# Kernel tuning notes

Measured on AMD Instinct MI355X. Metric: run time of the kernel, lower is better.

Reference implementation:

```python
import jax, jax.numpy as jnp
import numpy as np

T, N, HID = 128, 128, 64
H_, W_ = 8, 8
CONV_OUT = H_ * W_ * HID  # 4096
N_SUB = 5
A, B, C = 5, 3, 6          # subtask_space = task_space.nvec[0]
SUB_SIZE = A + B + C       # 14
N_G = A * B * C            # 90
STATE = N_SUB + SUB_SIZE + HID + SUB_SIZE + 1 + 1  # 99
D_IN = CONV_OUT + 3 * N_SUB  # 4111


def setup_inputs() -> dict:
    key = jax.random.key(0)
    ks = jax.random.split(key, 16)
    sc = 0.02
    obs = jax.random.normal(ks[0], (T, N, CONV_OUT), jnp.float32)
    task_type = jax.random.randint(ks[1], (T, N, N_SUB), 0, A).astype(jnp.float32)
    count = jax.random.randint(ks[2], (T, N, N_SUB), 1, B + 1).astype(jnp.float32)
    obj = jax.random.randint(ks[3], (T, N, N_SUB), 0, C).astype(jnp.float32)
    inp = jnp.concatenate([obs, task_type, count, obj], axis=-1)  # [T,N,4111]
    hx = jnp.zeros((1, N, STATE), jnp.float32)
    return {
        "input": inp,
        "hx": hx,
        "Wf": jax.random.normal(ks[4], (HID, CONV_OUT + 2 * SUB_SIZE + 1), jnp.float32) * sc,
        "bf": jnp.zeros((HID,), jnp.float32),
        "Wih": jax.random.normal(ks[5], (3 * HID, 2 * HID), jnp.float32) * sc,
        "bih": jnp.zeros((3 * HID,), jnp.float32),
        "bhh": jnp.zeros((3 * HID,), jnp.float32),
        "Wc": jax.random.normal(ks[6], (1, 2 * HID), jnp.float32) * sc,
        "bc": jnp.zeros((1,), jnp.float32),
        "Wl": jax.random.normal(ks[7], (3, HID), jnp.float32) * sc,
        "bl": jnp.zeros((3,), jnp.float32),
        "Wpi": jax.random.normal(ks[8], (N_G, HID + SUB_SIZE), jnp.float32) * sc,
        "bpi": jnp.zeros((N_G,), jnp.float32),
        "Wb": jax.random.normal(ks[9], (2, CONV_OUT + SUB_SIZE), jnp.float32) * sc,
        "bb": jnp.zeros((2,), jnp.float32),
    }


def _forward(input, hx, Wf, bf, Wih, bih, bhh, Wc, bc, Wl, bl, Wpi, bpi, Wb, bb):
    obs = input[..., :CONV_OUT]
    tt = input[..., CONV_OUT:CONV_OUT + N_SUB].astype(jnp.int32)
    cnt = input[..., CONV_OUT + N_SUB:CONV_OUT + 2 * N_SUB].astype(jnp.int32) - 1
    obj = input[..., CONV_OUT + 2 * N_SUB:].astype(jnp.int32)

    ea, eb, ec = jnp.eye(A, dtype=input.dtype), jnp.eye(B, dtype=input.dtype), jnp.eye(C, dtype=input.dtype)

    def embed(t1, t2, t3):
        return jnp.concatenate([ea[t1], eb[t2], ec[t3]], axis=-1)

    M = embed(tt[0], cnt[0], obj[0])  # [N, N_SUB, SUB_SIZE]

    # parse hidden state
    h0_all = hx[0]
    i0, i1, i2, i3, i4 = np.cumsum([N_SUB, SUB_SIZE, HID, SUB_SIZE, 1])
    p0, r0, h0, g0, b0 = (h0_all[:, :i0], h0_all[:, i0:i1], h0_all[:, i1:i2],
                          h0_all[:, i2:i3], h0_all[:, i3:i4])

    new_ep = jnp.all(hx == 0)
    p0 = jnp.where(new_ep, p0.at[:, 0].set(1.0), p0)
    r0 = jnp.where(new_ep, M[:, 0], r0)
    g0 = jnp.where(new_ep, M[:, 0], g0)

    bhr, bhz, bhn = jnp.split(bhh, 3)
    keys = jax.random.split(jax.random.key(42), input.shape[0])

    def step(carry, xs):
        p_, r_, h_, g_, bprev = carry
        x, k = xs
        s = jnp.concatenate([x, r_, g_, bprev], axis=-1) @ Wf.T + bf   # f (linear)
        sh = jnp.concatenate([s, h_], axis=-1)
        cg = jax.nn.sigmoid(sh @ Wc.T + bc)                             # [N,1] phi_update
        # GRUCell called with hidden=None -> zero hidden state
        gi = sh @ Wih.T + bih
        gr, gz, gn = jnp.split(gi, 3, axis=-1)
        rg = jax.nn.sigmoid(gr + bhr)
        z = jax.nn.sigmoid(gz + bhz)
        n = jnp.tanh(gn + rg * bhn)
        hnew = (1.0 - z) * n
        # shift attention: per-batch conv1d(p, l, padding=1)
        l = jax.nn.softmax(h_ @ Wl.T + bl, axis=-1)                     # [N,3]
        pp = jnp.pad(p_, ((0, 0), (1, 1)))
        pconv = pp[:, :-2] * l[:, :1] + pp[:, 1:-1] * l[:, 1:2] + pp[:, 2:] * l[:, 2:]
        rnew = jnp.einsum('nk,nks->ns', pconv, M)
        p = cg * pconv + (1.0 - cg) * p_
        r = cg * rnew + (1.0 - cg) * r_
        h = cg * hnew + (1.0 - cg) * h_
        # pi_theta categorical over prod(subtask_space)
        lg = jnp.concatenate([h, r], axis=-1) @ Wpi.T + bpi
        k1, k2 = jax.random.split(k)
        g_idx = jax.random.categorical(k1, lg)                          # [N]
        lp_g = jnp.take_along_axis(jax.nn.log_softmax(lg, axis=-1), g_idx[:, None], axis=1)
        t1 = g_idx // (B * C)
        rem = g_idx % (B * C)
        gemb = embed(t1, rem // C, rem % C)                             # [N, SUB_SIZE]
        g = cg * gemb + (1.0 - cg) * g_
        # beta categorical over 2
        lbeta = jnp.concatenate([x, g], axis=-1) @ Wb.T + bb
        b_idx = jax.random.categorical(k2, lbeta)
        lp_b = jnp.take_along_axis(jax.nn.log_softmax(lbeta, axis=-1), b_idx[:, None], axis=1)
        bflt = b_idx[:, None].astype(p.dtype)
        out = jnp.concatenate([p, r, h, g, bflt, lp_g + lp_b], axis=-1)  # [N, STATE]
        return (p, r, h, g, bflt), out

    _, outs = jax.lax.scan(step, (p0, r0, h0, g0, b0), (obs, keys))
    return outs  # [T, N, STATE]


def reference(input, hx, Wf, bf, Wih, bih, bhh, Wc, bc, Wl, bl, Wpi, bpi, Wb, bb):
    outs = _forward(input, hx, Wf, bf, Wih, bih, bhh, Wc, bc, Wl, bl, Wpi, bpi, Wb, bb)
    return outs, outs[-1]
```

## Files before the change

### kernel.cpp

```cpp
#include <hip/hip_runtime.h>
#include <stdint.h>
#include <math.h>

#define T_STEPS 128
#define NB      128
#define HID     64
#define CONVOUT 4096
#define NSUB    5
#define SUBSZ   14
#define NG      90
#define STATE   99
#define DIN     4111
#define WFCOLS  4125
#define WBCOLS  4110
#define NROWS   (T_STEPS * NB)
#define GIXST   193

#define NEGINFF (-3.0e38f)

typedef __attribute__((ext_vector_type(2))) float f32x2;

#define SEL5(a,b,c,d,e,ix) ((ix)==0?(a):(ix)==1?(b):(ix)==2?(c):(ix)==3?(d):(e))
#define SEL3(a,b,c,ix)     ((ix)==0?(a):(ix)==1?(b):(c))
#define SEL6(a,b,c,d,e,f,ix) ((ix)==0?(a):(ix)==1?(b):(ix)==2?(c):(ix)==3?(d):(ix)==4?(e):(f))
// ... 225 lines not shown
  float* o = GIx + (size_t)row * GIXST + i0;
  #pragma unroll
  for (int j = 0; j < 48; ++j) o[j] = acc[j];
  if (w == 3) o[48] = acc48;
}

__global__ void k_noise(double* __restrict__ Gg, double* __restrict__ Gb) {
  int b = blockIdx.x;
  int t = b / 9, c = b - t * 9;
  int tid = threadIdx.x;
  unsigned a, bk, k1a, k1b, k2a, k2b, o0, o1;
  tf2x32(0u, 42u, 0u, (unsigned)t, a, bk);
  if (c < 8) {
    tf2x32(a, bk, 0u, 0u, k1a, k1b);
    int i0 = c * 1440;
    for (int i = i0 + tid; i < i0 + 1440; i += 256) {
      tf2x32(k1a, k1b, 0u, (unsigned)i, o0, o1);
      Gg[(size_t)t * NB * NG + i] = bits_to_gumbel_d(o0 ^ o1);
    }
  } else {
    tf2x32(a, bk, 0u, 1u, k2a, k2b);
    tf2x32(k2a, k2b, 0u, (unsigned)tid, o0, o1);
    Gb[(size_t)t * NB * 2 + tid] = bits_to_gumbel_d(o0 ^ o1);
  }
}

__global__ __launch_bounds__(256, 1) void k_scan(
    const float* __restrict__ inp, const float* __restrict__ hx,
    const float* __restrict__ Wf,
    const float* __restrict__ Wih, const float* __restrict__ bih,
    const float* __restrict__ bhh, const float* __restrict__ Wc,
    const float* __restrict__ bc, const float* __restrict__ Wl,
    const float* __restrict__ bl, const float* __restrict__ Wpi,
    const float* __restrict__ bpi, const float* __restrict__ Wb,
    const float* __restrict__ bb,
    const float* __restrict__ GIx, const double* __restrict__ Xb,
    const double* __restrict__ Gg, const double* __restrict__ Gb,
    float* __restrict__ lgst, float* __restrict__ lbst,
    int* __restrict__ gidxst, int* __restrict__ bidxst,
    float* __restrict__ out) {
  const int n = blockIdx.x;
  const int tid = threadIdx.x;
  const int lane = tid & 63;
  const int w = __builtin_amdgcn_readfirstlane(tid >> 6);

  __shared__ __align__(16) float h_lds[64];
  __shared__ __align__(16) float gi_lds[192];
  __shared__ float pq_lds[4];
  __shared__ float cp_lds[2][8];
  __shared__ float pm_lds[3][2];
  __shared__ int   pidx_lds[3];
  __shared__ int   pub_i[4];
  __shared__ float pub_f[2];
  __shared__ int   nz_sh;
  __shared__ float ws_lds[29][64];
  __shared__ float rg0_lds[32];
  __shared__ int   ti_lds[16];

  const int i = tid - 64;
  const int oi = (w >= 1) ? (w - 1) * 30 + lane : 0;

  f32x2 wih_h[32];
  f32x2 wpi_p[32];
  float bihc = 0.f, bpi_r = 0.f;
  float Mg[14], V[5], WpiM[5];
  float m_b = 0.f, GI_r = 0.f, GI_g = 0.f, accR = 0.f, gihreg = 0.f;
  float gixA = 0.f;
  double gumA = 0.0, gumB = 0.0;
  #pragma unroll
  for (int j = 0; j < 14; ++j) Mg[j] = 0.f;
  #pragma unroll
  for (int k = 0; k < 5; ++k) { V[k] = 0.f; WpiM[k] = 0.f; }

  float rgbp = 0.f, hreg = 0.f;
  float mtr[5];
  float bhr_r = 0, bhz_r = 0, bhn_r = 0;
  float wc0 = 0, wc1 = 0, wl0 = 0, wl1 = 0, wl2 = 0;
  float bl0 = 0, bl1 = 0, bl2 = 0, bc0 = 0;
  float wbs0 = 0, wbs1 = 0;
  float kap[5], wg[14], wcB = 0.f;
  float cR = 0.f, cG = 0.f, CXa = 0.f;
  double S0 = 0.0, S1 = 0.0, bb0d = 0.0, bb1d = 0.0;
  double xb0 = 0.0, xb1 = 0.0, gb0 = 0.0, gb1 = 0.0;
  double xb0n = 0.0, xb1n = 0.0, gb0n = 0.0, gb1n = 0.0;
  int dsto = -1;
  int ttk[5], cnk[5], obk[5];
  float wfs[29];
  #pragma unroll
  for (int k = 0; k < 5; ++k) { mtr[k] = 0.f; kap[k] = 0.f; ttk[k] = 0; cnk[k] = 0; obk[k] = 0; }
  #pragma unroll
  for (int j = 0; j < 14; ++j) wg[j] = 0.f;
  #pragma unroll
  for (int k = 0; k < 29; ++k) wfs[k] = 0.f;

  if (tid == 0) nz_sh = 0;
  __syncthreads();
  {
    int any = 0;
    const float4* h4 = (const float4*)hx;
    for (int q = tid; q < (NB * STATE) / 4; q += 256) {
      float4 v = h4[q];
      any |= (v.x != 0.f) | (v.y != 0.f) | (v.z != 0.f) | (v.w != 0.f);
    }
    if (any) nz_sh = 1;
  }
  if (w == 0) {
    #pragma unroll
    for (int k = 0; k < 29; ++k) wfs[k] = Wf[(size_t)lane * WFCOLS + CONVOUT + k];
    bhr_r = bhh[lane]; bhz_r = bhh[64 + lane]; bhn_r = bhh[128 + lane];
    wc0 = Wc[lane]; wc1 = Wc[64 + lane]; bc0 = bc[0];
    wl0 = Wl[lane]; wl1 = Wl[64 + lane]; wl2 = Wl[128 + lane];
    bl0 = bl[0]; bl1 = bl[1]; bl2 = bl[2];
    bb0d = (double)bb[0]; bb1d = (double)bb[1];
    if (lane < 14) { wbs0 = Wb[CONVOUT + lane]; wbs1 = Wb[(size_t)WBCOLS + CONVOUT + lane]; }
    const float* r0 = inp + (size_t)n * DIN + CONVOUT;
    #pragma unroll
    for (int k = 0; k < 5; ++k) {
      int ttv = (int)r0[k], cntv = (int)r0[5 + k] - 1, objv = (int)r0[10 + k];
      ttk[k] = ttv; cnk[k] = cntv; obk[k] = objv;
      float v = 0.f;
      if (lane < 5)       v = (lane == ttv) ? 1.f : 0.f;
      else if (lane < 8)  v = ((lane - 5) == cntv) ? 1.f : 0.f;
      else if (lane < 14) v = ((lane - 8) == objv) ? 1.f : 0.f;
      mtr[k] = v;
      if (lane == 0) { ti_lds[k] = ttv; ti_lds[5 + k] = cntv; ti_lds[10 + k] = objv; }
    }
    int src = -1;
    if (lane < 14)       { dsto = 5 + lane;          src = dsto; }
    else if (lane < 28)  { dsto = 83 + (lane - 14);  src = dsto; }
    else if (lane == 28) { dsto = 97;                src = 97; }
    else if (lane < 34)  { dsto = lane - 29;         src = dsto; }
    rgbp = (src >= 0) ? hx[(size_t)n * STATE + src] : 0.f;
    hreg = hx[(size_t)n * STATE + 19 + lane];
  }
  __syncthreads();

  if (w == 0) {
    if (nz_sh == 0) {
      if (lane == 29) rgbp = 1.f;
      else if (lane < 14) rgbp = mtr[0];
      else if (lane >= 14 && lane < 28) {
        int j = lane - 14;
        rgbp = (j < 5) ? ((j == ttk[0]) ? 1.f : 0.f)
             : (j < 8) ? (((j - 5) == cnk[0]) ? 1.f : 0.f)
                       : (((j - 8) == obk[0]) ? 1.f : 0.f);
      }
    }
    #pragma unroll
    for (int j = 0; j < 29; ++j) ws_lds[j][lane] = wfs[j];
    if (lane < 28) rg0_lds[lane] = rgbp;
    if (lane == 28) { rg0_lds[28] = rgbp; pub_f[0] = rgbp; }
    h_lds[lane] = hreg;
    if (lane < 6) cp_lds[1][lane] = 0.f;
    if (lane < 3) pub_i[lane] = 0;
  }
  __syncthreads();

  if (w == 0) {
    #pragma unroll
    for (int k = 0; k < 5; ++k) {
      float wfrm = SEL5(wfs[0], wfs[1], wfs[2], wfs[3], wfs[4], ttk[k])
                 + SEL3(wfs[5], wfs[6], wfs[7], cnk[k])
                 + SEL6(wfs[8], wfs[9], wfs[10], wfs[11], wfs[12], wfs[13], obk[k]);
      kap[k] = dpp_sum_bcast(wc0 * wfrm);
    }
    #pragma unroll
    for (int j = 0; j < 14; ++j) wg[j] = dpp_sum_bcast(wc0 * wfs[14 + j]);
    wcB = dpp_sum_bcast(wc0 * wfs[28]);
    {
      float rs = 0.f, gs = 0.f;
      #pragma unroll
      for (int j = 0; j < 14; ++j) {
        rs = fmaf(wfs[j], rlane(rgbp, j), rs);
        gs = fmaf(wfs[14 + j], rlane(rgbp, 14 + j), gs);
      }
      cR = dpp_sum_bcast(wc0 * rs);
      cG = dpp_sum_bcast(wc0 * gs);
    }
    #pragma unroll
    for (int j = 0; j < 14; ++j) {
      double gv = (double)rlane(rgbp, 14 + j);
      S0 += gv * (double)rlane(wbs0, j);
      S1 += gv * (double)rlane(wbs1, j);
    }
    CXa = GIx[((size_t)0 * NB + n) * GIXST + 192];
    xb0 = Xb[(size_t)n * 2 + 0]; xb1 = Xb[(size_t)n * 2 + 1];
    gb0 = Gb[(size_t)n * 2 + 0]; gb1 = Gb[(size_t)n * 2 + 1];
    float p0 = wl0 * hreg, p1 = wl1 * hreg, p2 = wl2 * hreg, cah = wc1 * hreg;
    dpp_sum4(p0, p1, p2, cah);
    if (lane == 63) { pq_lds[0] = p0; pq_lds[1] = p1; pq_lds[2] = p2; pq_lds[3] = cah; }
  } else {
    float Mr[14];
    #pragma unroll
    for (int j = 0; j < 14; ++j) Mr[j] = 0.f;
    {
      float wsrow[64];
      {
        const f32x2* wr0 = (const f32x2*)&Wih[(size_t)i * 128];
        #pragma unroll
        for (int l2 = 0; l2 < 32; ++l2) { f32x2 v = wr0[l2]; wsrow[2*l2] = v.x; wsrow[2*l2+1] = v.y; }
      }
      #pragma unroll
      for (int l = 0; l < 64; ++l) {
        float wv = wsrow[l];
        #pragma unroll
        for (int j = 0; j < 14; ++j) {
          Mr[j] = fmaf(wv, ws_lds[j][l], Mr[j]);
          Mg[j] = fmaf(wv, ws_lds[14 + j][l], Mg[j]);
        }
        m_b = fmaf(wv, ws_lds[28][l], m_b);
      }
    }
    #pragma unroll
    for (int k = 0; k < 5; ++k) {
      int tt = ti_lds[k], cn = ti_lds[5 + k], ob = ti_lds[10 + k];
      V[k] = SEL5(Mr[0], Mr[1], Mr[2], Mr[3], Mr[4], tt)
           + SEL3(Mr[5], Mr[6], Mr[7], cn)
           + SEL6(Mr[8], Mr[9], Mr[10], Mr[11], Mr[12], Mr[13], ob);
    }
    GI_r = 0.f; GI_g = 0.f;
    #pragma unroll
    for (int j = 0; j < 14; ++j) {
      GI_r = fmaf(Mr[j], rg0_lds[j], GI_r);
      GI_g = fmaf(Mg[j], rg0_lds[14 + j], GI_g);
    }
    {
      const f32x2* wr = (const f32x2*)&Wih[(size_t)i * 128 + 64];
      #pragma unroll
      for (int k2 = 0; k2 < 32; ++k2) wih_h[k2] = wr[k2];
      bihc = bih[i];
    }
    if (lane < 30) {
      const f32x2* pr = (const f32x2*)&Wpi[(size_t)oi * 78];
      #pragma unroll
      for (int k2 = 0; k2 < 32; ++k2) wpi_p[k2] = pr[k2];
      bpi_r = bpi[oi];
      const float* wp = Wpi + (size_t)oi * 78 + 64;
      #pragma unroll
      for (int k = 0; k < 5; ++k)
        WpiM[k] = wp[ti_lds[k]] + wp[5 + ti_lds[5 + k]] + wp[8 + ti_lds[10 + k]];
      accR = 0.f;
      #pragma unroll
      for (int j = 0; j < 14; ++j) accR = fmaf(wp[j], rg0_lds[j], accR);
      gumA = Gg[(size_t)n * NG + oi];
    }
    gixA = GIx[((size_t)0 * NB + n) * GIXST + i];
    {
      const f32x2* hp = (const f32x2*)h_lds;
      f32x2 A = {bihc, 0.f}, B = {0.f, 0.f};
      #pragma unroll
      for (int k2 = 0; k2 < 32; k2 += 2) {
        f32x2 h0 = hp[k2], h1 = hp[k2 + 1];
        A.x = fmaf(wih_h[k2].x, h0.x, A.x);
        A.y = fmaf(wih_h[k2].y, h0.y, A.y);
        B.x = fmaf(wih_h[k2 + 1].x, h1.x, B.x);
        B.y = fmaf(wih_h[k2 + 1].y, h1.y, B.y);
      }
      gihreg = (A.x + A.y) + (B.x + B.y);
    }
  }
  __syncthreads();

  const size_t outF = (size_t)T_STEPS * NB * STATE;

  float cg = 0.f;
  double cgd = 0.0;

  #pragma unroll 1
  for (int t = 0; t < T_STEPS; ++t) {
    if (w == 0) {
      float P0 = pq_lds[0] + bl0, P1v = pq_lds[1] + bl1, P2v = pq_lds[2] + bl2;
      float cgaH = pq_lds[3];
      float mx = fmaxf(P0, fmaxf(P1v, P2v));
      float e0 = expf(P0 - mx), e1 = expf(P1v - mx), e2 = expf(P2v - mx);
      float se = e0 + e1 + e2;
      float l0 = e0 / se, l1 = e1 / se, l2 = e2 / se;
      float bprev = rlane(rgbp, 28);
      float cga = CXa + cR + cG + bprev * wcB + cgaH;
      cg = 1.f / (1.f + expf(-(cga + bc0)));
      cgd = (double)cg;
      float pv0 = rlane(rgbp, 29), pv1 = rlane(rgbp, 30), pv2 = rlane(rgbp, 31);
      float pv3 = rlane(rgbp, 32), pv4 = rlane(rgbp, 33);
      float pc0 = pv0 * l1 + pv1 * l2;
      float pc1 = pv0 * l0 + pv1 * l1 + pv2 * l2;
      float pc2 = pv1 * l0 + pv2 * l1 + pv3 * l2;
      float pc3 = pv2 * l0 + pv3 * l1 + pv4 * l2;
      float pc4 = pv3 * l0 + pv4 * l1;
      if (lane >= 29 && lane < 34) {
        float pcl = (lane == 29) ? pc0 : (lane == 30) ? pc1 : (lane == 31) ? pc2
                  : (lane == 32) ? pc3 : pc4;
        rgbp = cg * pcl + (1.f - cg) * rgbp;
      }
      if (lane < 14) {
        float rn2 = pc0 * mtr[0] + pc1 * mtr[1] + pc2 * mtr[2] + pc3 * mtr[3] + pc4 * mtr[4];
        rgbp = cg * rn2 + (1.f - cg) * rgbp;
      }
      cR = cg * (pc0 * kap[0] + pc1 * kap[1] + pc2 * kap[2] + pc3 * kap[3] + pc4 * kap[4])
         + (1.f - cg) * cR;
      if (lane == 0) {
        float* cp = cp_lds[t & 1];
        cp[0] = cg; cp[1] = pc0; cp[2] = pc1; cp[3] = pc2; cp[4] = pc3; cp[5] = pc4;
      }
    } else {
      const float* cp = cp_lds[(t + 1) & 1];
      float cgp = cp[0];
      float rmix = cp[1] * V[0] + cp[2] * V[1] + cp[3] * V[2] + cp[4] * V[3] + cp[5] * V[4];
      GI_r = cgp * rmix + (1.f - cgp) * GI_r;
      int pt1 = pub_i[0], pb1 = pub_i[1], pc1i = pub_i[2];
      float mgs = SEL5(Mg[0], Mg[1], Mg[2], Mg[3], Mg[4], pt1)
                + SEL3(Mg[5], Mg[6], Mg[7], pb1)
                + SEL6(Mg[8], Mg[9], Mg[10], Mg[11], Mg[12], Mg[13], pc1i);
      GI_g = cgp * mgs + (1.f - cgp) * GI_g;
      float bprev = pub_f[0];
      gi_lds[i] = gihreg + gixA + GI_r + GI_g + bprev * m_b;
    }
    bar_lds();

    if (w == 0) {
      float g0 = gi_lds[lane], g1 = gi_lds[64 + lane], g2 = gi_lds[128 + lane];
      float rg = 1.f / (1.f + expf(-(g0 + bhr_r)));
      float z  = 1.f / (1.f + expf(-(g1 + bhz_r)));
      float nn = tanhf(g2 + rg * bhn_r);
      hreg = cg * ((1.f - z) * nn) + (1.f - cg) * hreg;
      h_lds[lane] = hreg;
    } else {
      int tn = (t + 1 < T_STEPS) ? t + 1 : t;
      gixA = GIx[((size_t)tn * NB + n) * GIXST + i];
      if (lane < 30) gumB = Gg[(size_t)tn * NB * NG + (size_t)n * NG + oi];
    }
    bar_lds();

    if (w != 0) {
      const float* cp = cp_lds[t & 1];
      float cgc = cp[0];
      float vb = NEGINFF;
      if (lane < 30) {
        float rmx = cp[1] * WpiM[0] + cp[2] * WpiM[1] + cp[3] * WpiM[2]
                  + cp[4] * WpiM[3] + cp[5] * WpiM[4];
        accR = cgc * rmx + (1.f - cgc) * accR;
        const f32x2* hp = (const f32x2*)h_lds;
        f32x2 A = {bpi_r + accR, 0.f}, B = {0.f, 0.f};
        #pragma unroll
        for (int k2 = 0; k2 < 32; k2 += 2) {
          f32x2 h0 = hp[k2], h1 = hp[k2 + 1];
          A.x = fmaf(wpi_p[k2].x, h0.x, A.x);
          A.y = fmaf(wpi_p[k2].y, h0.y, A.y);
          B.x = fmaf(wpi_p[k2 + 1].x, h1.x, B.x);
          B.y = fmaf(wpi_p[k2 + 1].y, h1.y, B.y);
        }
        float lgv = (A.x + A.y) + (B.x + B.y);
        lgst[((size_t)t * NB + n) * NG + oi] = lgv;
        vb = (float)(gumA + (double)lgv);
      }
      gumA = gumB;
      float m1 = vb, m2 = NEGINFF;
      dpp_amax2(m1, m2);
      float M1w = rlane(m1, 63);
      unsigned long long bm = __ballot(vb == M1w);
      int il = __ffsll(bm) - 1;
      if (lane == 63) { pm_lds[w - 1][0] = m1; pm_lds[w - 1][1] = m2; pidx_lds[w - 1] = il; }
    } else {
      float p0 = wl0 * hreg, p1 = wl1 * hreg, p2 = wl2 * hreg, cah = wc1 * hreg;
      dpp_sum4(p0, p1, p2, cah);
      if (lane == 63) { pq_lds[0] = p0; pq_lds[1] = p1; pq_lds[2] = p2; pq_lds[3] = cah; }
      size_t rn = (size_t)t * NB + n;
      float* ob = out + rn * STATE;
      ob[19 + lane] = hreg;
      if (dsto >= 0 && (lane < 14 || lane >= 29)) ob[dsto] = rgbp;
      int tn = (t + 1 < T_STEPS) ? t + 1 : t;
      CXa = GIx[((size_t)tn * NB + n) * GIXST + 192];
      xb0n = Xb[((size_t)tn * NB + n) * 2 + 0];
      xb1n = Xb[((size_t)tn * NB + n) * 2 + 1];
      gb0n = Gb[((size_t)tn * NB + n) * 2 + 0];
      gb1n = Gb[((size_t)tn * NB + n) * 2 + 1];
    }
    bar_lds();

    if (w == 0) {
      float m1a = pm_lds[0][0], m2a = pm_lds[0][1];
      float m1b = pm_lds[1][0], m2b = pm_lds[1][1];
      float m1c = pm_lds[2][0], m2c = pm_lds[2][1];
      float M1 = fmaxf(m1a, fmaxf(m1b, m1c));
      float M2; int gidx;
      if (m1a == M1)      { M2 = fmaxf(m2a, fmaxf(m1b, m1c)); gidx = pidx_lds[0]; }
      else if (m1b == M1) { M2 = fmaxf(m2b, fmaxf(m1a, m1c)); gidx = 30 + pidx_lds[1]; }
      else                { M2 = fmaxf(m2c, fmaxf(m1a, m1b)); gidx = 60 + pidx_lds[2]; }
      if (M1 - M2 < 3e-5f) {
        double gum0s = Gg[(size_t)t * NB * NG + (size_t)n * NG + lane];
        double gum1s = (lane < 26) ? Gg[(size_t)t * NB * NG + (size_t)n * NG + 64 + lane] : 0.0;
        double e0d = (double)bpi[lane];
        double e1d = (lane < 26) ? (double)bpi[64 + lane] : -1.0e300;
        #pragma unroll 1
        for (int k = 0; k < 64; ++k) {
          double hv2 = (double)rlane(hreg, k);
          e0d = fma((double)Wpi[(size_t)lane * 78 + k], hv2, e0d);
          if (lane < 26) e1d = fma((double)Wpi[(size_t)(64 + lane) * 78 + k], hv2, e1d);
        }
        #pragma unroll 1
        for (int k = 0; k < 14; ++k) {
          double rv = (double)rlane(rgbp, k);
          e0d = fma((double)Wpi[(size_t)lane * 78 + 64 + k], rv, e0d);
          if (lane < 26) e1d = fma((double)Wpi[(size_t)(64 + lane) * 78 + 64 + k], rv, e1d);
        }
        double kk0 = e0d + gum0s;
        double kk1 = (lane < 26) ? e1d + gum1s : -1.0e300;
        double d1; int di;
        if (kk1 > kk0) { d1 = kk1; di = lane + 64; } else { d1 = kk0; di = lane; }
        #pragma unroll
        for (int off = 32; off; off >>= 1) {
          double od = __shfl_xor(d1, off, 64);
          int    oid = __shfl_xor(di, off, 64);
          if (od > d1 || (od == d1 && oid < di)) { d1 = od; di = oid; }
        }
        gidx = di;
      }
      int t1 = gidx / 18, rem = gidx - t1 * 18;
      int b1 = rem / 6, c1 = rem - b1 * 6;
      if (lane >= 14 && lane < 28) {
        int j = lane - 14;
        float ge = (j < 5) ? ((j == t1) ? 1.f : 0.f)
                 : (j < 8) ? (((j - 5) == b1) ? 1.f : 0.f)
                           : (((j - 8) == c1) ? 1.f : 0.f);
        rgbp = cg * ge + (1.f - cg) * rgbp;
      }
      float wgs = SEL5(wg[0], wg[1], wg[2], wg[3], wg[4], t1)
                + SEL3(wg[5], wg[6], wg[7], b1)
                + SEL6(wg[8], wg[9], wg[10], wg[11], wg[12], wg[13], c1);
      cG = cg * wgs + (1.f - cg) * cG;
      double u0 = (double)rlane(wbs0, t1) + (double)rlane(wbs0, 5 + b1) + (double)rlane(wbs0, 8 + c1);
      double u1 = (double)rlane(wbs1, t1) + (double)rlane(wbs1, 5 + b1) + (double)rlane(wbs1, 8 + c1);
      S0 = cgd * u0 + (1.0 - cgd) * S0;
      S1 = cgd * u1 + (1.0 - cgd) * S1;
      double lb0 = xb0 + bb0d + S0;
      double lb1 = xb1 + bb1d + S1;
      int bi = ((lb1 + gb1) > (lb0 + gb0)) ? 1 : 0;
      if (lane == 28) rgbp = (float)bi;
      size_t rn = (size_t)t * NB + n;
      float* ob = out + rn * STATE;
      if (dsto >= 0 && lane >= 14 && lane < 29) ob[dsto] = rgbp;
      if (lane == 0) {
        lbst[rn * 2 + 0] = (float)lb0; lbst[rn * 2 + 1] = (float)lb1;
        gidxst[rn] = gidx; bidxst[rn] = bi;
        pub_i[0] = t1; pub_i[1] = b1; pub_i[2] = c1;
      }
      if (lane == 28) pub_f[0] = rgbp;
      if (t == T_STEPS - 1) {
        float* of = out + outF + (size_t)n * STATE;
        if (dsto >= 0) of[dsto] = rgbp;
        of[19 + lane] = hreg;
      }
      xb0 = xb0n; xb1 = xb1n; gb0 = gb0n; gb1 = gb1n;
    } else {
      const f32x2* hp = (const f32x2*)h_lds;
      f32x2 A = {bihc, 0.f}, B = {0.f, 0.f};
      #pragma unroll
      for (int k2 = 0; k2 < 32; k2 += 2) {
        f32x2 h0 = hp[k2], h1 = hp[k2 + 1];
        A.x = fmaf(wih_h[k2].x, h0.x, A.x);
        A.y = fmaf(wih_h[k2].y, h0.y, A.y);
        B.x = fmaf(wih_h[k2 + 1].x, h1.x, B.x);
        B.y = fmaf(wih_h[k2 + 1].y, h1.y, B.y);
      }
      gihreg = (A.x + A.y) + (B.x + B.y);
    }
    bar_lds();
  }
}

__global__ __launch_bounds__(256) void k_lp(const float* __restrict__ lgst,
                                            const float* __restrict__ lbst,
                                            const int* __restrict__ gidxst,
                                            const int* __restrict__ bidxst,
                                            float* __restrict__ out) {
  int tid = threadIdx.x, lane = tid & 63, w = tid >> 6;
  size_t rn = (size_t)blockIdx.x * 4 + w;
  const float* lg = lgst + rn * NG;
  float v0 = lg[lane];
  float v1 = (lane < 26) ? lg[64 + lane] : -3.0e38f;
  float ml = fmaxf(v0, v1);
  #pragma unroll
  for (int off = 32; off; off >>= 1) ml = fmaxf(ml, __shfl_xor(ml, off, 64));
  float e = expf(v0 - ml) + ((lane < 26) ? expf(v1 - ml) : 0.f);
  #pragma unroll
  for (int off = 32; off; off >>= 1) e += __shfl_xor(e, off, 64);
  int gi = gidxst[rn];
  float lpg = (lg[gi] - ml) - logf(e);
  float lb0 = lbst[rn * 2 + 0], lb1 = lbst[rn * 2 + 1];
  int bi = bidxst[rn];
  float mx = fmaxf(lb0, lb1);
  float seb = expf(lb0 - mx) + expf(lb1 - mx);
  float lpb = ((bi ? lb1 : lb0) - mx) - logf(seb);
  if (lane == 0) {
    int t = (int)(rn / NB), n = (int)(rn % NB);
    float lp = lpg + lpb;
    out[rn * STATE + 98] = lp;
    if (t == T_STEPS - 1) out[(size_t)T_STEPS * NB * STATE + (size_t)n * STATE + 98] = lp;
  }
}

extern "C" void kernel_launch(void* const* d_in, const int* in_sizes, int n_in,
                              void* d_out, int out_size, void* d_ws, size_t ws_size,
                              hipStream_t stream) {
  const float* inp = (const float*)d_in[0];
  const float* hx  = (const float*)d_in[1];
  const float* Wf  = (const float*)d_in[2];
  const float* bf  = (const float*)d_in[3];
  const float* Wih = (const float*)d_in[4];
  const float* bih = (const float*)d_in[5];
  const float* bhh = (const float*)d_in[6];
  const float* Wc  = (const float*)d_in[7];
  const float* bc  = (const float*)d_in[8];
  const float* Wl  = (const float*)d_in[9];
  const float* bl  = (const float*)d_in[10];
  const float* Wpi = (const float*)d_in[11];
  const float* bpi = (const float*)d_in[12];
  const float* Wb  = (const float*)d_in[13];
  const float* bb  = (const float*)d_in[14];
  float* out = (float*)d_out;
// ... 30 lines not shown
```

Before: 940.6 us.

## Split recurrent loop into per-wave role loops and drop hx scan barrier

Restructures the sequential recurrence kernel so that wave 0 and the worker waves each run their own specialized time loop with matching barrier counts. Per-role state is scoped to its own branch, which is meant to cut register pressure and remove the per-step wave-uniform branching. The hx nonzero scan now runs in wave 0 only and uses a ballot instead of a shared flag, so one block-wide sync disappears. The risk is that the barrier sequences of the two loops fall out of step, which would deadlock or corrupt results, and the hx scan now runs on 64 threads instead of 256.

```diff
diff --git a/kernel.cpp b/kernel.cpp
--- a/kernel.cpp
+++ b/kernel.cpp
@@ -301,59 +301,38 @@
   __shared__ int   pidx_lds[3];
   __shared__ int   pub_i[4];
   __shared__ float pub_f[2];
-  __shared__ int   nz_sh;
   __shared__ float ws_lds[29][64];
   __shared__ float rg0_lds[32];
   __shared__ int   ti_lds[16];
 
-  const int i = tid - 64;
-  const int oi = (w >= 1) ? (w - 1) * 30 + lane : 0;
-
-  f32x2 wih_h[32];
-  f32x2 wpi_p[32];
-  float bihc = 0.f, bpi_r = 0.f;
-  float Mg[14], V[5], WpiM[5];
-  float m_b = 0.f, GI_r = 0.f, GI_g = 0.f, accR = 0.f, gihreg = 0.f;
-  float gixA = 0.f;
-  double gumA = 0.0, gumB = 0.0;
-  #pragma unroll
-  for (int j = 0; j < 14; ++j) Mg[j] = 0.f;
-  #pragma unroll
-  for (int k = 0; k < 5; ++k) { V[k] = 0.f; WpiM[k] = 0.f; }
-
-  float rgbp = 0.f, hreg = 0.f;
-  float mtr[5];
-  float bhr_r = 0, bhz_r = 0, bhn_r = 0;
-  float wc0 = 0, wc1 = 0, wl0 = 0, wl1 = 0, wl2 = 0;
-  float bl0 = 0, bl1 = 0, bl2 = 0, bc0 = 0;
-  float wbs0 = 0, wbs1 = 0;
-  float kap[5], wg[14], wcB = 0.f;
-  float cR = 0.f, cG = 0.f, CXa = 0.f;
-  double S0 = 0.0, S1 = 0.0, bb0d = 0.0, bb1d = 0.0;
-  double xb0 = 0.0, xb1 = 0.0, gb0 = 0.0, gb1 = 0.0;
-  double xb0n = 0.0, xb1n = 0.0, gb0n = 0.0, gb1n = 0.0;
-  int dsto = -1;
-  int ttk[5], cnk[5], obk[5];
-  float wfs[29];
-  #pragma unroll
-  for (int k = 0; k < 5; ++k) { mtr[k] = 0.f; kap[k] = 0.f; ttk[k] = 0; cnk[k] = 0; obk[k] = 0; }
-  #pragma unroll
-  for (int j = 0; j < 14; ++j) wg[j] = 0.f;
-  #pragma unroll
-  for (int k = 0; k < 29; ++k) wfs[k] = 0.f;
-
-  if (tid == 0) nz_sh = 0;
-  __syncthreads();
-  {
-    int any = 0;
-    const float4* h4 = (const float4*)hx;
-    for (int q = tid; q < (NB * STATE) / 4; q += 256) {
-      float4 v = h4[q];
-      any |= (v.x != 0.f) | (v.y != 0.f) | (v.z != 0.f) | (v.w != 0.f);
-    }
-    if (any) nz_sh = 1;
-  }
+  const size_t outF = (size_t)T_STEPS * NB * STATE;
+
   if (w == 0) {
+    float rgbp = 0.f, hreg = 0.f;
+    float mtr[5];
+    float bhr_r, bhz_r, bhn_r;
+    float wc0, wc1, wl0, wl1, wl2;
+    float bl0, bl1, bl2, bc0;
+    float wbs0 = 0.f, wbs1 = 0.f;
+    float kap[5], wg[14], wcB;
+    float cR, cG, CXa;
+    double S0 = 0.0, S1 = 0.0, bb0d, bb1d;
+    double xb0, xb1, gb0, gb1;
+    double xb0n, xb1n, gb0n, gb1n;
+    int dsto = -1;
+    int ttk[5], cnk[5], obk[5];
+    float wfs[29];
+
+    bool nz;
+    {
+      int any = 0;
+      const float4* h4 = (const float4*)hx;
+      for (int q = lane; q < (NB * STATE) / 4; q += 64) {
+        float4 v = h4[q];
+        any |= (v.x != 0.f) | (v.y != 0.f) | (v.z != 0.f) | (v.w != 0.f);
+      }
+      nz = (__ballot(any) != 0ULL);
+    }
     #pragma unroll
     for (int k = 0; k < 29; ++k) wfs[k] = Wf[(size_t)lane * WFCOLS + CONVOUT + k];
     bhr_r = bhh[lane]; bhz_r = bhh[64 + lane]; bhn_r = bhh[128 + lane];
@@ -362,30 +341,30 @@
     bl0 = bl[0]; bl1 = bl[1]; bl2 = bl[2];
     bb0d = (double)bb[0]; bb1d = (double)bb[1];
     if (lane < 14) { wbs0 = Wb[CONVOUT + lane]; wbs1 = Wb[(size_t)WBCOLS + CONVOUT + lane]; }
-    const float* r0 = inp + (size_t)n * DIN + CONVOUT;
-    #pragma unroll
-    for (int k = 0; k < 5; ++k) {
-      int ttv = (int)r0[k], cntv = (int)r0[5 + k] - 1, objv = (int)r0[10 + k];
-      ttk[k] = ttv; cnk[k] = cntv; obk[k] = objv;
-      float v = 0.f;
-      if (lane < 5)       v = (lane == ttv) ? 1.f : 0.f;
-      else if (lane < 8)  v = ((lane - 5) == cntv) ? 1.f : 0.f;
-      else if (lane < 14) v = ((lane - 8) == objv) ? 1.f : 0.f;
-      mtr[k] = v;
-      if (lane == 0) { ti_lds[k] = ttv; ti_lds[5 + k] = cntv; ti_lds[10 + k] = objv; }
-    }
-    int src = -1;
-    if (lane < 14)       { dsto = 5 + lane;          src = dsto; }
-    else if (lane < 28)  { dsto = 83 + (lane - 14);  src = dsto; }
-    else if (lane == 28) { dsto = 97;                src = 97; }
-    else if (lane < 34)  { dsto = lane - 29;         src = dsto; }
-    rgbp = (src >= 0) ? hx[(size_t)n * STATE + src] : 0.f;
-    hreg = hx[(size_t)n * STATE + 19 + lane];
-  }
-  __syncthreads();
-
-  if (w == 0) {
-    if (nz_sh == 0) {
+    {
+      const float* r0 = inp + (size_t)n * DIN + CONVOUT;
+      #pragma unroll
+      for (int k = 0; k < 5; ++k) {
+        int ttv = (int)r0[k], cntv = (int)r0[5 + k] - 1, objv = (int)r0[10 + k];
+        ttk[k] = ttv; cnk[k] = cntv; obk[k] = objv;
+        float v = 0.f;
+        if (lane < 5)       v = (lane == ttv) ? 1.f : 0.f;
+        else if (lane < 8)  v = ((lane - 5) == cntv) ? 1.f : 0.f;
+        else if (lane < 14) v = ((lane - 8) == objv) ? 1.f : 0.f;
+        mtr[k] = v;
+        if (lane == 0) { ti_lds[k] = ttv; ti_lds[5 + k] = cntv; ti_lds[10 + k] = objv; }
+      }
+    }
+    {
+      int src = -1;
+      if (lane < 14)       { dsto = 5 + lane;          src = dsto; }
+      else if (lane < 28)  { dsto = 83 + (lane - 14);  src = dsto; }
+      else if (lane == 28) { dsto = 97;                src = 97; }
+      else if (lane < 34)  { dsto = lane - 29;         src = dsto; }
+      rgbp = (src >= 0) ? hx[(size_t)n * STATE + src] : 0.f;
+      hreg = hx[(size_t)n * STATE + 19 + lane];
+    }
+    if (!nz) {
       if (lane == 29) rgbp = 1.f;
       else if (lane < 14) rgbp = mtr[0];
       else if (lane >= 14 && lane < 28) {
@@ -402,10 +381,9 @@
     h_lds[lane] = hreg;
     if (lane < 6) cp_lds[1][lane] = 0.f;
     if (lane < 3) pub_i[lane] = 0;
-  }
-  __syncthreads();
-
-  if (w == 0) {
+
+    bar_lds();
+
     #pragma unroll
     for (int k = 0; k < 5; ++k) {
       float wfrm = SEL5(wfs[0], wfs[1], wfs[2], wfs[3], wfs[4], ttk[k])
@@ -435,43 +413,213 @@
     CXa = GIx[((size_t)0 * NB + n) * GIXST + 192];
     xb0 = Xb[(size_t)n * 2 + 0]; xb1 = Xb[(size_t)n * 2 + 1];
     gb0 = Gb[(size_t)n * 2 + 0]; gb1 = Gb[(size_t)n * 2 + 1];
-    float p0 = wl0 * hreg, p1 = wl1 * hreg, p2 = wl2 * hreg, cah = wc1 * hreg;
-    dpp_sum4(p0, p1, p2, cah);
-    if (lane == 63) { pq_lds[0] = p0; pq_lds[1] = p1; pq_lds[2] = p2; pq_lds[3] = cah; }
+    xb0n = xb0; xb1n = xb1; gb0n = gb0; gb1n = gb1;
+    {
+      float p0 = wl0 * hreg, p1 = wl1 * hreg, p2 = wl2 * hreg, cah = wc1 * hreg;
+      dpp_sum4(p0, p1, p2, cah);
+      if (lane == 63) { pq_lds[0] = p0; pq_lds[1] = p1; pq_lds[2] = p2; pq_lds[3] = cah; }
+    }
+
+    bar_lds();
+
+    float cg = 0.f;
+    double cgd = 0.0;
+
+    #pragma unroll 1
+    for (int t = 0; t < T_STEPS; ++t) {
+      {
+        float P0 = pq_lds[0] + bl0, P1v = pq_lds[1] + bl1, P2v = pq_lds[2] + bl2;
+        float cgaH = pq_lds[3];
+        float mx = fmaxf(P0, fmaxf(P1v, P2v));
+        float e0 = expf(P0 - mx), e1 = expf(P1v - mx), e2 = expf(P2v - mx);
+        float se = e0 + e1 + e2;
+        float l0 = e0 / se, l1 = e1 / se, l2 = e2 / se;
+        float bprev = rlane(rgbp, 28);
+        float cga = CXa + cR + cG + bprev * wcB + cgaH;
+        cg = 1.f / (1.f + expf(-(cga + bc0)));
+        cgd = (double)cg;
+        float pv0 = rlane(rgbp, 29), pv1 = rlane(rgbp, 30), pv2 = rlane(rgbp, 31);
+        float pv3 = rlane(rgbp, 32), pv4 = rlane(rgbp, 33);
+        float pc0 = pv0 * l1 + pv1 * l2;
+        float pc1 = pv0 * l0 + pv1 * l1 + pv2 * l2;
+        float pc2 = pv1 * l0 + pv2 * l1 + pv3 * l2;
+        float pc3 = pv2 * l0 + pv3 * l1 + pv4 * l2;
+        float pc4 = pv3 * l0 + pv4 * l1;
+        if (lane >= 29 && lane < 34) {
+          float pcl = (lane == 29) ? pc0 : (lane == 30) ? pc1 : (lane == 31) ? pc2
+                    : (lane == 32) ? pc3 : pc4;
+          rgbp = cg * pcl + (1.f - cg) * rgbp;
+        }
+        if (lane < 14) {
+          float rn2 = pc0 * mtr[0] + pc1 * mtr[1] + pc2 * mtr[2] + pc3 * mtr[3] + pc4 * mtr[4];
+          rgbp = cg * rn2 + (1.f - cg) * rgbp;
+        }
+        cR = cg * (pc0 * kap[0] + pc1 * kap[1] + pc2 * kap[2] + pc3 * kap[3] + pc4 * kap[4])
+           + (1.f - cg) * cR;
+        if (lane == 0) {
+          float* cp = cp_lds[t & 1];
+          cp[0] = cg; cp[1] = pc0; cp[2] = pc1; cp[3] = pc2; cp[4] = pc3; cp[5] = pc4;
+        }
+      }
+      bar_lds();
+
+      {
+        float g0 = gi_lds[lane], g1 = gi_lds[64 + lane], g2 = gi_lds[128 + lane];
+        float rg = 1.f / (1.f + expf(-(g0 + bhr_r)));
+        float z  = 1.f / (1.f + expf(-(g1 + bhz_r)));
+        float nn = tanhf(g2 + rg * bhn_r);
+        hreg = cg * ((1.f - z) * nn) + (1.f - cg) * hreg;
+        h_lds[lane] = hreg;
+      }
+      bar_lds();
+
+      {
+        float p0 = wl0 * hreg, p1 = wl1 * hreg, p2 = wl2 * hreg, cah = wc1 * hreg;
+        dpp_sum4(p0, p1, p2, cah);
+        if (lane == 63) { pq_lds[0] = p0; pq_lds[1] = p1; pq_lds[2] = p2; pq_lds[3] = cah; }
+        size_t rn = (size_t)t * NB + n;
+        float* ob = out + rn * STATE;
+        ob[19 + lane] = hreg;
+        if (dsto >= 0 && (lane < 14 || lane >= 29)) ob[dsto] = rgbp;
+        int tn = (t + 1 < T_STEPS) ? t + 1 : t;
+        CXa = GIx[((size_t)tn * NB + n) * GIXST + 192];
+        xb0n = Xb[((size_t)tn * NB + n) * 2 + 0];
+        xb1n = Xb[((size_t)tn * NB + n) * 2 + 1];
+        gb0n = Gb[((size_t)tn * NB + n) * 2 + 0];
+        gb1n = Gb[((size_t)tn * NB + n) * 2 + 1];
+      }
+      bar_lds();
+
+      {
+        float m1a = pm_lds[0][0], m2a = pm_lds[0][1];
+        float m1b = pm_lds[1][0], m2b = pm_lds[1][1];
+        float m1c = pm_lds[2][0], m2c = pm_lds[2][1];
+        float M1 = fmaxf(m1a, fmaxf(m1b, m1c));
+        float M2; int gidx;
+        if (m1a == M1)      { M2 = fmaxf(m2a, fmaxf(m1b, m1c)); gidx = pidx_lds[0]; }
+        else if (m1b == M1) { M2 = fmaxf(m2b, fmaxf(m1a, m1c)); gidx = 30 + pidx_lds[1]; }
+        else                { M2 = fmaxf(m2c, fmaxf(m1a, m1b)); gidx = 60 + pidx_lds[2]; }
+        if (M1 - M2 < 3e-5f) {
+          double gum0s = Gg[(size_t)t * NB * NG + (size_t)n * NG + lane];
+          double gum1s = (lane < 26) ? Gg[(size_t)t * NB * NG + (size_t)n * NG + 64 + lane] : 0.0;
+          double e0d = (double)bpi[lane];
+          double e1d = (lane < 26) ? (double)bpi[64 + lane] : -1.0e300;
+          #pragma unroll 1
+          for (int k = 0; k < 64; ++k) {
+            double hv2 = (double)rlane(hreg, k);
+            e0d = fma((double)Wpi[(size_t)lane * 78 + k], hv2, e0d);
+            if (lane < 26) e1d = fma((double)Wpi[(size_t)(64 + lane) * 78 + k], hv2, e1d);
+          }
+          #pragma unroll 1
+          for (int k = 0; k < 14; ++k) {
+            double rv = (double)rlane(rgbp, k);
+            e0d = fma((double)Wpi[(size_t)lane * 78 + 64 + k], rv, e0d);
+            if (lane < 26) e1d = fma((double)Wpi[(size_t)(64 + lane) * 78 + 64 + k], rv, e1d);
+          }
+          double kk0 = e0d + gum0s;
+          double kk1 = (lane < 26) ? e1d + gum1s : -1.0e300;
+          double d1; int di;
+          if (kk1 > kk0) { d1 = kk1; di = lane + 64; } else { d1 = kk0; di = lane; }
+          #pragma unroll
+          for (int off = 32; off; off >>= 1) {
+            double od = __shfl_xor(d1, off, 64);
+            int    oid = __shfl_xor(di, off, 64);
+            if (od > d1 || (od == d1 && oid < di)) { d1 = od; di = oid; }
+          }
+          gidx = di;
+        }
+        int t1 = gidx / 18, rem = gidx - t1 * 18;
+        int b1 = rem / 6, c1 = rem - b1 * 6;
+        if (lane >= 14 && lane < 28) {
+          int j = lane - 14;
+          float ge = (j < 5) ? ((j == t1) ? 1.f : 0.f)
+                   : (j < 8) ? (((j - 5) == b1) ? 1.f : 0.f)
+                             : (((j - 8) == c1) ? 1.f : 0.f);
+          rgbp = cg * ge + (1.f - cg) * rgbp;
+        }
+        float wgs = SEL5(wg[0], wg[1], wg[2], wg[3], wg[4], t1)
+                  + SEL3(wg[5], wg[6], wg[7], b1)
+                  + SEL6(wg[8], wg[9], wg[10], wg[11], wg[12], wg[13], c1);
+        cG = cg * wgs + (1.f - cg) * cG;
+        double u0 = (double)rlane(wbs0, t1) + (double)rlane(wbs0, 5 + b1) + (double)rlane(wbs0, 8 + c1);
+        double u1 = (double)rlane(wbs1, t1) + (double)rlane(wbs1, 5 + b1) + (double)rlane(wbs1, 8 + c1);
+        S0 = cgd * u0 + (1.0 - cgd) * S0;
+        S1 = cgd * u1 + (1.0 - cgd) * S1;
+        double lb0 = xb0 + bb0d + S0;
+        double lb1 = xb1 + bb1d + S1;
+        int bi = ((lb1 + gb1) > (lb0 + gb0)) ? 1 : 0;
+        if (lane == 28) rgbp = (float)bi;
+        size_t rn = (size_t)t * NB + n;
+        float* ob = out + rn * STATE;
+        if (dsto >= 0 && lane >= 14 && lane < 29) ob[dsto] = rgbp;
+        if (lane == 0) {
+          lbst[rn * 2 + 0] = (float)lb0; lbst[rn * 2 + 1] = (float)lb1;
+          gidxst[rn] = gidx; bidxst[rn] = bi;
+          pub_i[0] = t1; pub_i[1] = b1; pub_i[2] = c1;
+        }
+        if (lane == 28) pub_f[0] = rgbp;
+        if (t == T_STEPS - 1) {
+          float* of = out + outF + (size_t)n * STATE;
+          if (dsto >= 0) of[dsto] = rgbp;
+          of[19 + lane] = hreg;
+        }
+        xb0 = xb0n; xb1 = xb1n; gb0 = gb0n; gb1 = gb1n;
+      }
+      bar_lds();
+    }
   } else {
-    float Mr[14];
-    #pragma unroll
-    for (int j = 0; j < 14; ++j) Mr[j] = 0.f;
+    const int i = tid - 64;
+    const int oi = (w - 1) * 30 + lane;
+
+    f32x2 wih_h[32];
+    f32x2 wpi_p[32];
+    float bihc, bpi_r = 0.f;
+    float Mg[14], V[5], WpiM[5];
+    float m_b = 0.f, GI_r = 0.f, GI_g = 0.f, accR = 0.f, gihreg;
+    float gixA;
+    double gumA = 0.0, gumB = 0.0;
+    #pragma unroll
+    for (int j = 0; j < 14; ++j) Mg[j] = 0.f;
+    #pragma unroll
+    for (int k = 0; k < 5; ++k) WpiM[k] = 0.f;
+
+    bar_lds();
+
     {
-      float wsrow[64];
+      float Mr[14];
+      #pragma unroll
+      for (int j = 0; j < 14; ++j) Mr[j] = 0.f;
       {
-        const f32x2* wr0 = (const f32x2*)&Wih[(size_t)i * 128];
+        float wsrow[64];
+        {
+          const f32x2* wr0 = (const f32x2*)&Wih[(size_t)i * 128];
+          #pragma unroll
+          for (int l2 = 0; l2 < 32; ++l2) { f32x2 v = wr0[l2]; wsrow[2*l2] = v.x; wsrow[2*l2+1] = v.y; }
+        }
         #pragma unroll
-        for (int l2 = 0; l2 < 32; ++l2) { f32x2 v = wr0[l2]; wsrow[2*l2] = v.x; wsrow[2*l2+1] = v.y; }
-      }
-      #pragma unroll
-      for (int l = 0; l < 64; ++l) {
-        float wv = wsrow[l];
-        #pragma unroll
-        for (int j = 0; j < 14; ++j) {
-          Mr[j] = fmaf(wv, ws_lds[j][l], Mr[j]);
-          Mg[j] = fmaf(wv, ws_lds[14 + j][l], Mg[j]);
-        }
-        m_b = fmaf(wv, ws_lds[28][l], m_b);
-      }
-    }
-    #pragma unroll
-    for (int k = 0; k < 5; ++k) {
-      int tt = ti_lds[k], cn = ti_lds[5 + k], ob = ti_lds[10 + k];
-      V[k] = SEL5(Mr[0], Mr[1], Mr[2], Mr[3], Mr[4], tt)
-           + SEL3(Mr[5], Mr[6], Mr[7], cn)
-           + SEL6(Mr[8], Mr[9], Mr[10], Mr[11], Mr[12], Mr[13], ob);
-    }
-    GI_r = 0.f; GI_g = 0.f;
-    #pragma unroll
-    for (int j = 0; j < 14; ++j) {
-      GI_r = fmaf(Mr[j], rg0_lds[j], GI_r);
-      GI_g = fmaf(Mg[j], rg0_lds[14 + j], GI_g);
+        for (int l = 0; l < 64; ++l) {
+          float wv = wsrow[l];
+          #pragma unroll
+          for (int j = 0; j < 14; ++j) {
+            Mr[j] = fmaf(wv, ws_lds[j][l], Mr[j]);
+            Mg[j] = fmaf(wv, ws_lds[14 + j][l], Mg[j]);
+          }
+          m_b = fmaf(wv, ws_lds[28][l], m_b);
+        }
+      }
+      #pragma unroll
+      for (int k = 0; k < 5; ++k) {
+        int tt = ti_lds[k], cn = ti_lds[5 + k], ob = ti_lds[10 + k];
+        V[k] = SEL5(Mr[0], Mr[1], Mr[2], Mr[3], Mr[4], tt)
+             + SEL3(Mr[5], Mr[6], Mr[7], cn)
+             + SEL6(Mr[8], Mr[9], Mr[10], Mr[11], Mr[12], Mr[13], ob);
+      }
+      GI_r = 0.f; GI_g = 0.f;
+      #pragma unroll
+      for (int j = 0; j < 14; ++j) {
+        GI_r = fmaf(Mr[j], rg0_lds[j], GI_r);
+        GI_g = fmaf(Mg[j], rg0_lds[14 + j], GI_g);
+      }
     }
     {
       const f32x2* wr = (const f32x2*)&Wih[(size_t)i * 128 + 64];
@@ -507,212 +655,80 @@
       }
       gihreg = (A.x + A.y) + (B.x + B.y);
     }
-  }
-  __syncthreads();
-
-  const size_t outF = (size_t)T_STEPS * NB * STATE;
-
-  float cg = 0.f;
-  double cgd = 0.0;
-
-  #pragma unroll 1
-  for (int t = 0; t < T_STEPS; ++t) {
-    if (w == 0) {
-      float P0 = pq_lds[0] + bl0, P1v = pq_lds[1] + bl1, P2v = pq_lds[2] + bl2;
-      float cgaH = pq_lds[3];
-      float mx = fmaxf(P0, fmaxf(P1v, P2v));
-      float e0 = expf(P0 - mx), e1 = expf(P1v - mx), e2 = expf(P2v - mx);
-      float se = e0 + e1 + e2;
-      float l0 = e0 / se, l1 = e1 / se, l2 = e2 / se;
-      float bprev = rlane(rgbp, 28);
-      float cga = CXa + cR + cG + bprev * wcB + cgaH;
-      cg = 1.f / (1.f + expf(-(cga + bc0)));
-      cgd = (double)cg;
-      float pv0 = rlane(rgbp, 29), pv1 = rlane(rgbp, 30), pv2 = rlane(rgbp, 31);
-      float pv3 = rlane(rgbp, 32), pv4 = rlane(rgbp, 33);
-      float pc0 = pv0 * l1 + pv1 * l2;
-      float pc1 = pv0 * l0 + pv1 * l1 + pv2 * l2;
-      float pc2 = pv1 * l0 + pv2 * l1 + pv3 * l2;
-      float pc3 = pv2 * l0 + pv3 * l1 + pv4 * l2;
-      float pc4 = pv3 * l0 + pv4 * l1;
-      if (lane >= 29 && lane < 34) {
-        float pcl = (lane == 29) ? pc0 : (lane == 30) ? pc1 : (lane == 31) ? pc2
-                  : (lane == 32) ? pc3 : pc4;
-        rgbp = cg * pcl + (1.f - cg) * rgbp;
-      }
-      if (lane < 14) {
-        float rn2 = pc0 * mtr[0] + pc1 * mtr[1] + pc2 * mtr[2] + pc3 * mtr[3] + pc4 * mtr[4];
-        rgbp = cg * rn2 + (1.f - cg) * rgbp;
-      }
-      cR = cg * (pc0 * kap[0] + pc1 * kap[1] + pc2 * kap[2] + pc3 * kap[3] + pc4 * kap[4])
-         + (1.f - cg) * cR;
-      if (lane == 0) {
-        float* cp = cp_lds[t & 1];
-        cp[0] = cg; cp[1] = pc0; cp[2] = pc1; cp[3] = pc2; cp[4] = pc3; cp[5] = pc4;
-      }
-    } else {
-      const float* cp = cp_lds[(t + 1) & 1];
-      float cgp = cp[0];
-      float rmix = cp[1] * V[0] + cp[2] * V[1] + cp[3] * V[2] + cp[4] * V[3] + cp[5] * V[4];
-      GI_r = cgp * rmix + (1.f - cgp) * GI_r;
-      int pt1 = pub_i[0], pb1 = pub_i[1], pc1i = pub_i[2];
-      float mgs = SEL5(Mg[0], Mg[1], Mg[2], Mg[3], Mg[4], pt1)
-                + SEL3(Mg[5], Mg[6], Mg[7], pb1)
-                + SEL6(Mg[8], Mg[9], Mg[10], Mg[11], Mg[12], Mg[13], pc1i);
-      GI_g = cgp * mgs + (1.f - cgp) * GI_g;
-      float bprev = pub_f[0];
-      gi_lds[i] = gihreg + gixA + GI_r + GI_g + bprev * m_b;
-    }
+
     bar_lds();
 
-    if (w == 0) {
-      float g0 = gi_lds[lane], g1 = gi_lds[64 + lane], g2 = gi_lds[128 + lane];
-      float rg = 1.f / (1.f + expf(-(g0 + bhr_r)));
-      float z  = 1.f / (1.f + expf(-(g1 + bhz_r)));
-      float nn = tanhf(g2 + rg * bhn_r);
-      hreg = cg * ((1.f - z) * nn) + (1.f - cg) * hreg;
-      h_lds[lane] = hreg;
-    } else {
-      int tn = (t + 1 < T_STEPS) ? t + 1 : t;
-      gixA = GIx[((size_t)tn * NB + n) * GIXST + i];
-      if (lane < 30) gumB = Gg[(size_t)tn * NB * NG + (size_t)n * NG + oi];
-    }
-    bar_lds();
-
-    if (w != 0) {
-      const float* cp = cp_lds[t & 1];
-      float cgc = cp[0];
-      float vb = NEGINFF;
-      if (lane < 30) {
-        float rmx = cp[1] * WpiM[0] + cp[2] * WpiM[1] + cp[3] * WpiM[2]
-                  + cp[4] * WpiM[3] + cp[5] * WpiM[4];
-        accR = cgc * rmx + (1.f - cgc) * accR;
+    #pragma unroll 1
+    for (int t = 0; t < T_STEPS; ++t) {
+      {
+        const float* cp = cp_lds[(t + 1) & 1];
+        float cgp = cp[0];
+        float rmix = cp[1] * V[0] + cp[2] * V[1] + cp[3] * V[2] + cp[4] * V[3] + cp[5] * V[4];
+        GI_r = cgp * rmix + (1.f - cgp) * GI_r;
+        int pt1 = pub_i[0], pb1 = pub_i[1], pc1i = pub_i[2];
+        float mgs = SEL5(Mg[0], Mg[1], Mg[2], Mg[3], Mg[4], pt1)
+                  + SEL3(Mg[5], Mg[6], Mg[7], pb1)
+                  + SEL6(Mg[8], Mg[9], Mg[10], Mg[11], Mg[12], Mg[13], pc1i);
+        GI_g = cgp * mgs + (1.f - cgp) * GI_g;
+        float bprev = pub_f[0];
+        gi_lds[i] = gihreg + gixA + GI_r + GI_g + bprev * m_b;
+      }
+      bar_lds();
+
+      {
+        int tn = (t + 1 < T_STEPS) ? t + 1 : t;
+        gixA = GIx[((size_t)tn * NB + n) * GIXST + i];
+        if (lane < 30) gumB = Gg[(size_t)tn * NB * NG + (size_t)n * NG + oi];
+      }
+      bar_lds();
+
+      {
+        const float* cp = cp_lds[t & 1];
+        float cgc = cp[0];
+        float vb = NEGINFF;
+        if (lane < 30) {
+          float rmx = cp[1] * WpiM[0] + cp[2] * WpiM[1] + cp[3] * WpiM[2]
+                    + cp[4] * WpiM[3] + cp[5] * WpiM[4];
+          accR = cgc * rmx + (1.f - cgc) * accR;
+          const f32x2* hp = (const f32x2*)h_lds;
+          f32x2 A = {bpi_r + accR, 0.f}, B = {0.f, 0.f};
+          #pragma unroll
+          for (int k2 = 0; k2 < 32; k2 += 2) {
+            f32x2 h0 = hp[k2], h1 = hp[k2 + 1];
+            A.x = fmaf(wpi_p[k2].x, h0.x, A.x);
+            A.y = fmaf(wpi_p[k2].y, h0.y, A.y);
+            B.x = fmaf(wpi_p[k2 + 1].x, h1.x, B.x);
+            B.y = fmaf(wpi_p[k2 + 1].y, h1.y, B.y);
+          }
+          float lgv = (A.x + A.y) + (B.x + B.y);
+          lgst[((size_t)t * NB + n) * NG + oi] = lgv;
+          vb = (float)(gumA + (double)lgv);
+        }
+        gumA = gumB;
+        float m1 = vb, m2 = NEGINFF;
+        dpp_amax2(m1, m2);
+        float M1w = rlane(m1, 63);
+        unsigned long long bm = __ballot(vb == M1w);
+        int il = __ffsll(bm) - 1;
+        if (lane == 63) { pm_lds[w - 1][0] = m1; pm_lds[w - 1][1] = m2; pidx_lds[w - 1] = il; }
+      }
+      bar_lds();
+
+      {
         const f32x2* hp = (const f32x2*)h_lds;
-        f32x2 A = {bpi_r + accR, 0.f}, B = {0.f, 0.f};
+        f32x2 A = {bihc, 0.f}, B = {0.f, 0.f};
         #pragma unroll
         for (int k2 = 0; k2 < 32; k2 += 2) {
           f32x2 h0 = hp[k2], h1 = hp[k2 + 1];
-          A.x = fmaf(wpi_p[k2].x, h0.x, A.x);
-          A.y = fmaf(wpi_p[k2].y, h0.y, A.y);
-          B.x = fmaf(wpi_p[k2 + 1].x, h1.x, B.x);
-          B.y = fmaf(wpi_p[k2 + 1].y, h1.y, B.y);
-        }
-        float lgv = (A.x + A.y) + (B.x + B.y);
-        lgst[((size_t)t * NB + n) * NG + oi] = lgv;
-        vb = (float)(gumA + (double)lgv);
-      }
-      gumA = gumB;
-      float m1 = vb, m2 = NEGINFF;
-      dpp_amax2(m1, m2);
-      float M1w = rlane(m1, 63);
-      unsigned long long bm = __ballot(vb == M1w);
-      int il = __ffsll(bm) - 1;
-      if (lane == 63) { pm_lds[w - 1][0] = m1; pm_lds[w - 1][1] = m2; pidx_lds[w - 1] = il; }
-    } else {
-      float p0 = wl0 * hreg, p1 = wl1 * hreg, p2 = wl2 * hreg, cah = wc1 * hreg;
-      dpp_sum4(p0, p1, p2, cah);
-      if (lane == 63) { pq_lds[0] = p0; pq_lds[1] = p1; pq_lds[2] = p2; pq_lds[3] = cah; }
-      size_t rn = (size_t)t * NB + n;
-      float* ob = out + rn * STATE;
-      ob[19 + lane] = hreg;
-      if (dsto >= 0 && (lane < 14 || lane >= 29)) ob[dsto] = rgbp;
-      int tn = (t + 1 < T_STEPS) ? t + 1 : t;
-      CXa = GIx[((size_t)tn * NB + n) * GIXST + 192];
-      xb0n = Xb[((size_t)tn * NB + n) * 2 + 0];
-      xb1n = Xb[((size_t)tn * NB + n) * 2 + 1];
-      gb0n = Gb[((size_t)tn * NB + n) * 2 + 0];
-      gb1n = Gb[((size_t)tn * NB + n) * 2 + 1];
-    }
-    bar_lds();
-
-    if (w == 0) {
-      float m1a = pm_lds[0][0], m2a = pm_lds[0][1];
-      float m1b = pm_lds[1][0], m2b = pm_lds[1][1];
-      float m1c = pm_lds[2][0], m2c = pm_lds[2][1];
-      float M1 = fmaxf(m1a, fmaxf(m1b, m1c));
-      float M2; int gidx;
-      if (m1a == M1)      { M2 = fmaxf(m2a, fmaxf(m1b, m1c)); gidx = pidx_lds[0]; }
-      else if (m1b == M1) { M2 = fmaxf(m2b, fmaxf(m1a, m1c)); gidx = 30 + pidx_lds[1]; }
-      else                { M2 = fmaxf(m2c, fmaxf(m1a, m1b)); gidx = 60 + pidx_lds[2]; }
-      if (M1 - M2 < 3e-5f) {
-        double gum0s = Gg[(size_t)t * NB * NG + (size_t)n * NG + lane];
-        double gum1s = (lane < 26) ? Gg[(size_t)t * NB * NG + (size_t)n * NG + 64 + lane] : 0.0;
-        double e0d = (double)bpi[lane];
-        double e1d = (lane < 26) ? (double)bpi[64 + lane] : -1.0e300;
-        #pragma unroll 1
-        for (int k = 0; k < 64; ++k) {
-          double hv2 = (double)rlane(hreg, k);
-          e0d = fma((double)Wpi[(size_t)lane * 78 + k], hv2, e0d);
-          if (lane < 26) e1d = fma((double)Wpi[(size_t)(64 + lane) * 78 + k], hv2, e1d);
-        }
-        #pragma unroll 1
-        for (int k = 0; k < 14; ++k) {
-          double rv = (double)rlane(rgbp, k);
-          e0d = fma((double)Wpi[(size_t)lane * 78 + 64 + k], rv, e0d);
-          if (lane < 26) e1d = fma((double)Wpi[(size_t)(64 + lane) * 78 + 64 + k], rv, e1d);
-        }
-        double kk0 = e0d + gum0s;
-        double kk1 = (lane < 26) ? e1d + gum1s : -1.0e300;
-        double d1; int di;
-        if (kk1 > kk0) { d1 = kk1; di = lane + 64; } else { d1 = kk0; di = lane; }
-        #pragma unroll
-        for (int off = 32; off; off >>= 1) {
-          double od = __shfl_xor(d1, off, 64);
-          int    oid = __shfl_xor(di, off, 64);
-          if (od > d1 || (od == d1 && oid < di)) { d1 = od; di = oid; }
-        }
-        gidx = di;
-      }
-      int t1 = gidx / 18, rem = gidx - t1 * 18;
-      int b1 = rem / 6, c1 = rem - b1 * 6;
-      if (lane >= 14 && lane < 28) {
-        int j = lane - 14;
-        float ge = (j < 5) ? ((j == t1) ? 1.f : 0.f)
-                 : (j < 8) ? (((j - 5) == b1) ? 1.f : 0.f)
-                           : (((j - 8) == c1) ? 1.f : 0.f);
-        rgbp = cg * ge + (1.f - cg) * rgbp;
-      }
-      float wgs = SEL5(wg[0], wg[1], wg[2], wg[3], wg[4], t1)
-                + SEL3(wg[5], wg[6], wg[7], b1)
-                + SEL6(wg[8], wg[9], wg[10], wg[11], wg[12], wg[13], c1);
-      cG = cg * wgs + (1.f - cg) * cG;
-      double u0 = (double)rlane(wbs0, t1) + (double)rlane(wbs0, 5 + b1) + (double)rlane(wbs0, 8 + c1);
-      double u1 = (double)rlane(wbs1, t1) + (double)rlane(wbs1, 5 + b1) + (double)rlane(wbs1, 8 + c1);
-      S0 = cgd * u0 + (1.0 - cgd) * S0;
-      S1 = cgd * u1 + (1.0 - cgd) * S1;
-      double lb0 = xb0 + bb0d + S0;
-      double lb1 = xb1 + bb1d + S1;
-      int bi = ((lb1 + gb1) > (lb0 + gb0)) ? 1 : 0;
-      if (lane == 28) rgbp = (float)bi;
-      size_t rn = (size_t)t * NB + n;
-      float* ob = out + rn * STATE;
-      if (dsto >= 0 && lane >= 14 && lane < 29) ob[dsto] = rgbp;
-      if (lane == 0) {
-        lbst[rn * 2 + 0] = (float)lb0; lbst[rn * 2 + 1] = (float)lb1;
-        gidxst[rn] = gidx; bidxst[rn] = bi;
-        pub_i[0] = t1; pub_i[1] = b1; pub_i[2] = c1;
-      }
-      if (lane == 28) pub_f[0] = rgbp;
-      if (t == T_STEPS - 1) {
-        float* of = out + outF + (size_t)n * STATE;
-        if (dsto >= 0) of[dsto] = rgbp;
-        of[19 + lane] = hreg;
-      }
-      xb0 = xb0n; xb1 = xb1n; gb0 = gb0n; gb1 = gb1n;
-    } else {
-      const f32x2* hp = (const f32x2*)h_lds;
-      f32x2 A = {bihc, 0.f}, B = {0.f, 0.f};
-      #pragma unroll
-      for (int k2 = 0; k2 < 32; k2 += 2) {
-        f32x2 h0 = hp[k2], h1 = hp[k2 + 1];
-        A.x = fmaf(wih_h[k2].x, h0.x, A.x);
-        A.y = fmaf(wih_h[k2].y, h0.y, A.y);
-        B.x = fmaf(wih_h[k2 + 1].x, h1.x, B.x);
-        B.y = fmaf(wih_h[k2 + 1].y, h1.y, B.y);
-      }
-      gihreg = (A.x + A.y) + (B.x + B.y);
-    }
-    bar_lds();
+          A.x = fmaf(wih_h[k2].x, h0.x, A.x);
+          A.y = fmaf(wih_h[k2].y, h0.y, A.y);
+          B.x = fmaf(wih_h[k2 + 1].x, h1.x, B.x);
+          B.y = fmaf(wih_h[k2 + 1].y, h1.y, B.y);
+        }
+        gihreg = (A.x + A.y) + (B.x + B.y);
+      }
+      bar_lds();
+    }
   }
 }
 
```

Measured after the change: 904.6 us. 3.8% less time.
